# Kernel optimization log

Hardware: AMD Instinct MI355X
Metric: run time of the kernel (lower is better)

The kernel has to match this reference:

```python
import jax, jax.numpy as jnp
import numpy as np

OCC_THRESHOLD = 0.5  # occupancy-bitfield stand-in: cell occupied if grid value > 0.5
T_CLAMP = 1e10


def setup_inputs() -> dict:
    key = jax.random.key(0)
    k1, k2, k3 = jax.random.split(key, 3)
    R = 65536
    # origins inside the scene box [-1,1]^3 (uniform in [-0.5,0.5]^3)
    rays_o = jax.random.uniform(k1, (R, 3), dtype=jnp.float32) - 0.5
    d = jax.random.normal(k2, (R, 3), dtype=jnp.float32)
    rays_d = d / jnp.linalg.norm(d, axis=-1, keepdims=True)
    aabb = jnp.array([[-1.0, -1.0, -1.0], [1.0, 1.0, 1.0]], dtype=jnp.float32)
    density_grid = jax.random.uniform(k3, (1, 128, 128, 128), dtype=jnp.float32)
    return {"rays_o": rays_o, "rays_d": rays_d, "aabb": aabb,
            "density_grid": density_grid, "num_samples": 128}


def reference(rays_o, rays_d, aabb, density_grid, num_samples):
    R = rays_o.shape[0]
    S = int(num_samples)
    aabb_min, aabb_max = aabb[0], aabb[1]

    # ---- ray-AABB intersection (slab test), matching nerfactory_cuda.ray_aabb_intersect ----
    inv_d = 1.0 / rays_d
    t0 = (aabb_min - rays_o) * inv_d  # [R,3]
    t1 = (aabb_max - rays_o) * inv_d
    tn = jnp.max(jnp.minimum(t0, t1), axis=-1)
    tf = jnp.min(jnp.maximum(t0, t1), axis=-1)
    tn = jnp.maximum(tn, 0.0)
    miss = tf <= tn
    t_min = jnp.minimum(jnp.where(miss, T_CLAMP, tn), T_CLAMP)  # [R]
    t_max = jnp.minimum(jnp.where(miss, T_CLAMP, tf), T_CLAMP)  # [R]

    # ---- raymarching: S uniform steps in [t_min, t_max], keep occupied cells ----
    dt = jnp.where(miss, 0.0, (t_max - t_min) / S)  # [R]
    i = jnp.arange(S, dtype=rays_o.dtype)
    starts = t_min[:, None] + i * dt[:, None]        # [R,S]
    ends = starts + dt[:, None]
    t_mid = 0.5 * (starts + ends)
    pos = rays_o[:, None, :] + rays_d[:, None, :] * t_mid[..., None]  # [R,S,3]

    res = density_grid.shape[-1]
    u = (pos - aabb_min) / (aabb_max - aabb_min)  # normalized [0,1]
    cell = jnp.clip(jnp.floor(u * res).astype(jnp.int32), 0, res - 1)
    occ = density_grid[0, cell[..., 0], cell[..., 1], cell[..., 2]] > OCC_THRESHOLD
    valid = occ & (~miss[:, None]) & (dt[:, None] > 0)  # [R,S]

    # ---- stream compaction into packed buffer (fixed capacity R*S) ----
    total = R * S
    flat_valid = valid.reshape(-1)
    excl = jnp.cumsum(flat_valid.astype(jnp.int32)) - flat_valid.astype(jnp.int32)
    scatter_idx = jnp.where(flat_valid, excl, total)  # invalid -> dummy slot

    origins_b = jnp.broadcast_to(rays_o[:, None, :], (R, S, 3))
    dirs_b = jnp.broadcast_to(rays_d[:, None, :], (R, S, 3))
    vals = jnp.concatenate(
        [origins_b, dirs_b, starts[..., None], ends[..., None]], axis=-1
    ).reshape(total, 8)
    packed = jnp.zeros((total + 1, 8), dtype=vals.dtype).at[scatter_idx].set(vals)[:total]

    counts = valid.sum(axis=-1).astype(jnp.int32)        # samples per ray
    ray_start = jnp.cumsum(counts) - counts              # exclusive cumsum
    packed_info = jnp.stack([ray_start, counts], axis=-1)  # [R,2]

    # packed columns: origins(0:3), dirs(3:6), starts(6), ends(7)
    return packed, packed_info, t_min, t_max
```

## Files before the change

### kernel.cpp

```cpp
#include <hip/hip_runtime.h>

#define SAMPLES 128
#define GRID_RES 128

typedef unsigned long long u64;

__device__ __forceinline__ void slab_test(
    float ox, float oy, float oz, float dx, float dy, float dz,
    float a0, float a1, float a2, float b0, float b1, float b2,
    float& tmin, float& tmax, float& dtv, bool& miss)
{
    float ix = __fdiv_rn(1.0f, dx);
    float iy = __fdiv_rn(1.0f, dy);
    float iz = __fdiv_rn(1.0f, dz);
    float t0x = __fmul_rn(__fsub_rn(a0, ox), ix);
    float t1x = __fmul_rn(__fsub_rn(b0, ox), ix);
    float t0y = __fmul_rn(__fsub_rn(a1, oy), iy);
    float t1y = __fmul_rn(__fsub_rn(b1, oy), iy);
    float t0z = __fmul_rn(__fsub_rn(a2, oz), iz);
    float t1z = __fmul_rn(__fsub_rn(b2, oz), iz);
    float tn = fmaxf(fmaxf(fminf(t0x, t1x), fminf(t0y, t1y)), fminf(t0z, t1z));
    float tf = fminf(fminf(fmaxf(t0x, t1x), fmaxf(t0y, t1y)), fmaxf(t0z, t1z));
    tn = fmaxf(tn, 0.0f);
    miss = (tf <= tn);
    tmin = miss ? 1e10f : fminf(tn, 1e10f);
    tmax = miss ? 1e10f : fminf(tf, 1e10f);
    dtv  = miss ? 0.0f : __fmul_rn(__fsub_rn(tmax, tmin), 0.0078125f);
}

__global__ __launch_bounds__(256) void k_prep(
    const float* __restrict__ grid, u64* __restrict__ bits,
    const float* __restrict__ ro, const float* __restrict__ rd,
    const float* __restrict__ aabb,
    float* __restrict__ out_tmin, float* __restrict__ out_tmax,
    float* __restrict__ wtmin, float* __restrict__ wdt,
    unsigned* __restrict__ ctr, int R, int nbb)
{
    int b = blockIdx.x;
    int tid = threadIdx.x;
    if (b < nbb) {
        int m = b * 256 + tid;
        int BZ = m & 31, BY = (m >> 5) & 31, BX = m >> 10;
        u64 word = 0;
        #pragma unroll
        for (int i = 0; i < 4; ++i) {
            #pragma unroll
            for (int j = 0; j < 4; ++j) {
                const float4 v = *(const float4*)(
                    grid + (((size_t)(BX * 4 + i) * GRID_RES + (BY * 4 + j))
                            * GRID_RES + BZ * 4));
                int base = (i << 4) | (j << 2);
                if (v.x > 0.5f) word |= (1ull << (base + 0));
                if (v.y > 0.5f) word |= (1ull << (base + 1));
                if (v.z > 0.5f) word |= (1ull << (base + 2));
                if (v.w > 0.5f) word |= (1ull << (base + 3));
            }
        }
        bits[m] = word;
        return;
    }
    int r = (b - nbb) * 256 + tid;
    if (b == nbb && tid == 0) *ctr = 0u;
    if (r >= R) return;
    float ox = ro[3 * r + 0], oy = ro[3 * r + 1], oz = ro[3 * r + 2];
    float dx = rd[3 * r + 0], dy = rd[3 * r + 1], dz = rd[3 * r + 2];
    float a0 = aabb[0], a1 = aabb[1], a2 = aabb[2];
    float b0 = aabb[3], b1 = aabb[4], b2 = aabb[5];
    float tmin, tmax, dtv; bool miss;
    slab_test(ox, oy, oz, dx, dy, dz, a0, a1, a2, b0, b1, b2,
              tmin, tmax, dtv, miss);
    out_tmin[r] = tmin;
    out_tmax[r] = tmax;
    wtmin[r] = tmin;
    wdt[r]  = dtv;
}

__device__ __forceinline__ float norm_coord(float p, float a, float e)
{
    if (e == 2.0f)
        return __fmul_rn(__fmul_rn(__fsub_rn(p, a), 0.5f), (float)GRID_RES);
    return __fmul_rn(__fdiv_rn(__fsub_rn(p, a), e), (float)GRID_RES);
}

__device__ __forceinline__ bool sample_occ(
    int s, float tmin, float dtv,
    float ox, float oy, float oz, float dx, float dy, float dz,
    float a0, float a1, float a2, float e0, float e1, float e2,
    const u64* __restrict__ bits)
{
    float fs    = (float)s;
    float start = __fadd_rn(tmin, __fmul_rn(fs, dtv));
    float end   = __fadd_rn(start, dtv);
    float tmid  = __fmul_rn(0.5f, __fadd_rn(start, end));
    float px = __fadd_rn(ox, __fmul_rn(dx, tmid));
    float py = __fadd_rn(oy, __fmul_rn(dy, tmid));
    float pz = __fadd_rn(oz, __fmul_rn(dz, tmid));
    float ux = norm_coord(px, a0, e0);
    float uy = norm_coord(py, a1, e1);
    float uz = norm_coord(pz, a2, e2);
    int cx = min(max((int)floorf(ux), 0), GRID_RES - 1);
    int cy = min(max((int)floorf(uy), 0), GRID_RES - 1);
    int cz = min(max((int)floorf(uz), 0), GRID_RES - 1);
    int m  = (((cx >> 2) << 5) | (cy >> 2)) * 32 + (cz >> 2);
    int bb = ((cx & 3) << 4) | ((cy & 3) << 2) | (cz & 3);
    return (bits[m] >> bb) & 1ull;
}

__global__ __launch_bounds__(256) void k_pass1(
    const float* __restrict__ ro, const float* __restrict__ rd,
    const float* __restrict__ aabb, const u64* __restrict__ bits,
    const float* __restrict__ wtmin, const float* __restrict__ wdt,
    u64* __restrict__ wmask, int R)
{
    int tid  = threadIdx.x;
    int lane = tid & 63;
    int ray  = blockIdx.x * 4 + (tid >> 6);
    if (ray >= R) return;
    int rayu = __builtin_amdgcn_readfirstlane(ray);

    float tmin = wtmin[rayu];
    float dtv  = wdt[rayu];

    bool vlo = false, vhi = false;
    if (dtv > 0.0f) {
        float ox = ro[3 * rayu + 0], oy = ro[3 * rayu + 1], oz = ro[3 * rayu + 2];
        float dx = rd[3 * rayu + 0], dy = rd[3 * rayu + 1], dz = rd[3 * rayu + 2];
        float a0 = aabb[0], a1 = aabb[1], a2 = aabb[2];
        float e0 = __fsub_rn(aabb[3], a0);
        float e1 = __fsub_rn(aabb[4], a1);
        float e2 = __fsub_rn(aabb[5], a2);
        vlo = sample_occ(lane,      tmin, dtv, ox, oy, oz, dx, dy, dz,
                         a0, a1, a2, e0, e1, e2, bits);
        vhi = sample_occ(lane + 64, tmin, dtv, ox, oy, oz, dx, dy, dz,
                         a0, a1, a2, e0, e1, e2, bits);
    }

    u64 mlo = __ballot(vlo);
    u64 mhi = __ballot(vhi);
    if (lane == 0) {
        ulonglong2 v; v.x = mlo; v.y = mhi;
        *(ulonglong2*)&wmask[(size_t)ray * 2] = v;
    }
}

__global__ __launch_bounds__(1024) void k_scan(
    const u64* __restrict__ wmask, unsigned* __restrict__ lpre,
    unsigned* __restrict__ bsum, unsigned* __restrict__ boff,
    unsigned* __restrict__ wtotal, unsigned* __restrict__ ctr,
    int R, int nb)
{
    int r    = blockIdx.x * 1024 + threadIdx.x;
    int lane = threadIdx.x & 63;
    int wv   = threadIdx.x >> 6;

    unsigned c = 0;
    if (r < R)
        c = (unsigned)__popcll(wmask[2 * r]) + (unsigned)__popcll(wmask[2 * r + 1]);

    unsigned inc = c;
    for (int o = 1; o < 64; o <<= 1) {
        unsigned v = __shfl_up(inc, o, 64);
        if (lane >= o) inc += v;
    }

    __shared__ unsigned sw[16];
    __shared__ unsigned sdone;
    if (lane == 63) sw[wv] = inc;
    __syncthreads();
    if (wv == 0) {
        unsigned v = (lane < 16) ? sw[lane] : 0u;
        unsigned iv = v;
        for (int o = 1; o < 16; o <<= 1) {
            unsigned t2 = __shfl_up(iv, o, 64);
            if (lane >= o) iv += t2;
        }
        if (lane < 16) sw[lane] = iv - v;
    }
    __syncthreads();

    unsigned excl = sw[wv] + (inc - c);
    if (r < R) lpre[r] = excl;

    if (threadIdx.x == 1023) {
        atomicExch(&bsum[blockIdx.x], excl + c);
        __threadfence();
        sdone = atomicAdd(ctr, 1u);
    }
    __syncthreads();
    if (sdone == (unsigned)(nb - 1)) {
        __threadfence();
        if (threadIdx.x < 64) {
            int t = threadIdx.x;
            unsigned v = (t < nb) ? atomicAdd(&bsum[t], 0u) : 0u;
            unsigned iv = v;
            for (int o = 1; o < 64; o <<= 1) {
                unsigned u = __shfl_up(iv, o, 64);
                if (t >= o) iv += u;
            }
            if (t < nb) boff[t] = iv - v;
            if (t == 63) *wtotal = iv;
        }
    }
}

__global__ __launch_bounds__(256) void k_pack(
    const float* __restrict__ ro, const float* __restrict__ rd,
    const u64* __restrict__ wmask,
    const unsigned* __restrict__ lpre, const unsigned* __restrict__ boff,
    const float* __restrict__ wtmin, const float* __restrict__ wdt,
    const unsigned* __restrict__ wtotal,
    float* __restrict__ packed, float* __restrict__ info, int R)
{
    __shared__ unsigned sbuf[4][64 * 9];

    int tid  = threadIdx.x;
    int wv   = tid >> 6;
    int lane = tid & 63;
    int gid  = blockIdx.x * 256 + tid;
    int ray  = gid >> 7;
    int s    = gid & 127;
    int s0   = s & 64;
    int rayu = __builtin_amdgcn_readfirstlane(ray);

    u64 mlo = wmask[2 * rayu];
    u64 mhi = wmask[2 * rayu + 1];
    u64 mw  = s0 ? mhi : mlo;
    unsigned nv = (unsigned)__popcll(mw);
    unsigned wave_below = (unsigned)__popcll(mw & ((1ull << lane) - 1ull));
    bool valid = (mw >> lane) & 1ull;
    unsigned rank = valid ? wave_below : nv + ((unsigned)lane - wave_below);

    unsigned wstart = boff[rayu >> 10] + lpre[rayu];
    unsigned vbase  = wstart + (s0 ? (unsigned)__popcll(mlo) : 0u);
    unsigned wtot   = *wtotal;
    unsigned gid0   = (unsigned)(gid - lane);
    unsigned tbase  = wtot + gid0 - vbase;

    if (s == 0) {
        unsigned cnt = (unsigned)__popcll(mlo) + (unsigned)__popcll(mhi);
        info[2 * ray]     = (float)wstart;
        info[2 * ray + 1] = (float)cnt;
    }

    unsigned d0 = 0u, d1 = 0u, d2 = 0u, d3 = 0u, d4 = 0u, d5 = 0u, d6 = 0u, d7 = 0u;
    if (valid) {
        float tmin  = wtmin[rayu];
        float dtv   = wdt[rayu];
        float fs    = (float)s;
        float start = __fadd_rn(tmin, __fmul_rn(fs, dtv));
        float end   = __fadd_rn(start, dtv);
        d0 = __float_as_uint(ro[3 * rayu + 0]);
        d1 = __float_as_uint(ro[3 * rayu + 1]);
        d2 = __float_as_uint(ro[3 * rayu + 2]);
        d3 = __float_as_uint(rd[3 * rayu + 0]);
        d4 = __float_as_uint(rd[3 * rayu + 1]);
        d5 = __float_as_uint(rd[3 * rayu + 2]);
        d6 = __float_as_uint(start);
        d7 = __float_as_uint(end);
    }
    unsigned* row = &sbuf[wv][rank * 9];
    row[0] = d0; row[1] = d1; row[2] = d2; row[3] = d3;
    row[4] = d4; row[5] = d5; row[6] = d6; row[7] = d7;

    __syncthreads();

    #pragma unroll
    for (int b = 0; b < 2; ++b) {
        unsigned f = (unsigned)(b * 64 + lane);
        unsigned k = f >> 1;
        unsigned p = f & 1u;
        unsigned dest = (k < nv) ? (vbase + k) : (tbase + (k - nv));
        const unsigned* src = &sbuf[wv][k * 9 + p * 4];
        float4 val = make_float4(__uint_as_float(src[0]), __uint_as_float(src[1]),
                                 __uint_as_float(src[2]), __uint_as_float(src[3]));
        *(float4*)(packed + (size_t)dest * 8 + p * 4) = val;
    }
}

extern "C" void kernel_launch(void* const* d_in, const int* in_sizes, int n_in,
                              void* d_out, int out_size, void* d_ws, size_t ws_size,
                              hipStream_t stream)
{
    const float* ro   = (const float*)d_in[0];
    const float* rd   = (const float*)d_in[1];
    const float* aabb = (const float*)d_in[2];
    const float* grid = (const float*)d_in[3];

    int R = in_sizes[0] / 3;
    size_t total = (size_t)R * SAMPLES;
    int nb = (R + 1023) / 1024;
    int nbricks = 32 * 32 * 32;
    int nbb = nbricks / 256;
    int nrb = (R + 255) / 256;

    float* out    = (float*)d_out;
    float* packed = out;
    float* info   = out + total * 8;
    float* otmin  = info + (size_t)2 * R;
    float* otmax  = otmin + R;

    char* w = (char*)d_ws;
    u64* wmask       = (u64*)w;
    float* wtmin     = (float*)(w + (size_t)R * 16);
    float* wdt       = wtmin + R;
    unsigned* lpre   = (unsigned*)(wdt + R);
    unsigned* bsum   = lpre + R;
    unsigned* boff   = bsum + 64;
    unsigned* wtotal = boff + 64;
    unsigned* ctr    = wtotal + 1;
    u64* bits        = (u64*)(wtotal + 63);

    k_prep<<<nbb + nrb, 256, 0, stream>>>(grid, bits, ro, rd, aabb,
                                          otmin, otmax, wtmin, wdt, ctr, R, nbb);
    int b1 = (R + 3) / 4;
    k_pass1<<<b1, 256, 0, stream>>>(ro, rd, aabb, bits, wtmin, wdt, wmask, R);
    k_scan<<<nb, 1024, 0, stream>>>(wmask, lpre, bsum, boff, wtotal, ctr, R, nb);
    int b3 = (int)(total / 256);
    k_pack<<<b3, 256, 0, stream>>>(ro, rd, wmask, lpre, boff, wtmin, wdt,
                                   wtotal, packed, info, R);
}
```

Measured before the change: 75.82 us.

## Fuse occupancy sampling pass with the per-ray count scan kernel

Merges the ray-sampling kernel and the scan kernel into a single launch. Each 1024-thread block now handles 16 rays, one per wave, and computes the ray counts directly from the ballot masks instead of re-reading them. The block sums then feed a last-block decoupled scan over 4096 block totals, with each thread handling four entries. This removes a kernel launch and the round trip of the masks through global memory. In exchange the final single-block scan is larger and there is more atomic-counter traffic across many blocks.

```diff
diff --git a/kernel.cpp b/kernel.cpp
--- a/kernel.cpp
+++ b/kernel.cpp
@@ -106,66 +106,51 @@
     return (bits[m] >> bb) & 1ull;
 }
 
-__global__ __launch_bounds__(256) void k_pass1(
+__global__ __launch_bounds__(1024) void k_pass1(
     const float* __restrict__ ro, const float* __restrict__ rd,
     const float* __restrict__ aabb, const u64* __restrict__ bits,
     const float* __restrict__ wtmin, const float* __restrict__ wdt,
-    u64* __restrict__ wmask, int R)
-{
-    int tid  = threadIdx.x;
-    int lane = tid & 63;
-    int ray  = blockIdx.x * 4 + (tid >> 6);
-    if (ray >= R) return;
-    int rayu = __builtin_amdgcn_readfirstlane(ray);
-
-    float tmin = wtmin[rayu];
-    float dtv  = wdt[rayu];
-
-    bool vlo = false, vhi = false;
-    if (dtv > 0.0f) {
-        float ox = ro[3 * rayu + 0], oy = ro[3 * rayu + 1], oz = ro[3 * rayu + 2];
-        float dx = rd[3 * rayu + 0], dy = rd[3 * rayu + 1], dz = rd[3 * rayu + 2];
-        float a0 = aabb[0], a1 = aabb[1], a2 = aabb[2];
-        float e0 = __fsub_rn(aabb[3], a0);
-        float e1 = __fsub_rn(aabb[4], a1);
-        float e2 = __fsub_rn(aabb[5], a2);
-        vlo = sample_occ(lane,      tmin, dtv, ox, oy, oz, dx, dy, dz,
-                         a0, a1, a2, e0, e1, e2, bits);
-        vhi = sample_occ(lane + 64, tmin, dtv, ox, oy, oz, dx, dy, dz,
-                         a0, a1, a2, e0, e1, e2, bits);
-    }
-
-    u64 mlo = __ballot(vlo);
-    u64 mhi = __ballot(vhi);
-    if (lane == 0) {
-        ulonglong2 v; v.x = mlo; v.y = mhi;
-        *(ulonglong2*)&wmask[(size_t)ray * 2] = v;
-    }
-}
-
-__global__ __launch_bounds__(1024) void k_scan(
-    const u64* __restrict__ wmask, unsigned* __restrict__ lpre,
+    u64* __restrict__ wmask, unsigned* __restrict__ lpre,
     unsigned* __restrict__ bsum, unsigned* __restrict__ boff,
     unsigned* __restrict__ wtotal, unsigned* __restrict__ ctr,
     int R, int nb)
 {
-    int r    = blockIdx.x * 1024 + threadIdx.x;
-    int lane = threadIdx.x & 63;
-    int wv   = threadIdx.x >> 6;
+    int tid  = threadIdx.x;
+    int lane = tid & 63;
+    int wv   = tid >> 6;
+    int ray  = blockIdx.x * 16 + wv;
+    bool act = (ray < R);
 
     unsigned c = 0;
-    if (r < R)
-        c = (unsigned)__popcll(wmask[2 * r]) + (unsigned)__popcll(wmask[2 * r + 1]);
-
-    unsigned inc = c;
-    for (int o = 1; o < 64; o <<= 1) {
-        unsigned v = __shfl_up(inc, o, 64);
-        if (lane >= o) inc += v;
+    if (act) {
+        int rayu = __builtin_amdgcn_readfirstlane(ray);
+        float tmin = wtmin[rayu];
+        float dtv  = wdt[rayu];
+        bool vlo = false, vhi = false;
+        if (dtv > 0.0f) {
+            float ox = ro[3 * rayu + 0], oy = ro[3 * rayu + 1], oz = ro[3 * rayu + 2];
+            float dx = rd[3 * rayu + 0], dy = rd[3 * rayu + 1], dz = rd[3 * rayu + 2];
+            float a0 = aabb[0], a1 = aabb[1], a2 = aabb[2];
+            float e0 = __fsub_rn(aabb[3], a0);
+            float e1 = __fsub_rn(aabb[4], a1);
+            float e2 = __fsub_rn(aabb[5], a2);
+            vlo = sample_occ(lane,      tmin, dtv, ox, oy, oz, dx, dy, dz,
+                             a0, a1, a2, e0, e1, e2, bits);
+            vhi = sample_occ(lane + 64, tmin, dtv, ox, oy, oz, dx, dy, dz,
+                             a0, a1, a2, e0, e1, e2, bits);
+        }
+        u64 mlo = __ballot(vlo);
+        u64 mhi = __ballot(vhi);
+        c = (unsigned)__popcll(mlo) + (unsigned)__popcll(mhi);
+        if (lane == 0) {
+            ulonglong2 v; v.x = mlo; v.y = mhi;
+            *(ulonglong2*)&wmask[(size_t)ray * 2] = v;
+        }
     }
 
     __shared__ unsigned sw[16];
     __shared__ unsigned sdone;
-    if (lane == 63) sw[wv] = inc;
+    if (lane == 0) sw[wv] = c;
     __syncthreads();
     if (wv == 0) {
         unsigned v = (lane < 16) ? sw[lane] : 0u;
@@ -177,29 +162,49 @@
         if (lane < 16) sw[lane] = iv - v;
     }
     __syncthreads();
-
-    unsigned excl = sw[wv] + (inc - c);
-    if (r < R) lpre[r] = excl;
-
-    if (threadIdx.x == 1023) {
-        atomicExch(&bsum[blockIdx.x], excl + c);
+    if (act && lane == 0) lpre[ray] = sw[wv];
+
+    if (tid == 960) {
+        atomicExch(&bsum[blockIdx.x], sw[15] + c);
         __threadfence();
         sdone = atomicAdd(ctr, 1u);
     }
     __syncthreads();
     if (sdone == (unsigned)(nb - 1)) {
         __threadfence();
-        if (threadIdx.x < 64) {
-            int t = threadIdx.x;
-            unsigned v = (t < nb) ? atomicAdd(&bsum[t], 0u) : 0u;
+        const int per = 4;
+        int base = tid * per;
+        unsigned v0 = 0, v1 = 0, v2 = 0, v3 = 0;
+        if (base + 0 < nb) v0 = atomicAdd(&bsum[base + 0], 0u);
+        if (base + 1 < nb) v1 = atomicAdd(&bsum[base + 1], 0u);
+        if (base + 2 < nb) v2 = atomicAdd(&bsum[base + 2], 0u);
+        if (base + 3 < nb) v3 = atomicAdd(&bsum[base + 3], 0u);
+        unsigned S = v0 + v1 + v2 + v3;
+
+        unsigned inc = S;
+        for (int o = 1; o < 64; o <<= 1) {
+            unsigned t2 = __shfl_up(inc, o, 64);
+            if (lane >= o) inc += t2;
+        }
+        __shared__ unsigned sw2[16];
+        if (lane == 63) sw2[wv] = inc;
+        __syncthreads();
+        if (wv == 0) {
+            unsigned v = (lane < 16) ? sw2[lane] : 0u;
             unsigned iv = v;
-            for (int o = 1; o < 64; o <<= 1) {
-                unsigned u = __shfl_up(iv, o, 64);
-                if (t >= o) iv += u;
+            for (int o = 1; o < 16; o <<= 1) {
+                unsigned t2 = __shfl_up(iv, o, 64);
+                if (lane >= o) iv += t2;
             }
-            if (t < nb) boff[t] = iv - v;
-            if (t == 63) *wtotal = iv;
-        }
+            if (lane < 16) sw2[lane] = iv - v;
+        }
+        __syncthreads();
+        unsigned run = sw2[wv] + (inc - S);
+        if (base + 0 < nb) { boff[base + 0] = run; run += v0; }
+        if (base + 1 < nb) { boff[base + 1] = run; run += v1; }
+        if (base + 2 < nb) { boff[base + 2] = run; run += v2; }
+        if (base + 3 < nb) { boff[base + 3] = run; run += v3; }
+        if (tid == 1023) *wtotal = run;
     }
 }
 
@@ -230,7 +235,7 @@
     bool valid = (mw >> lane) & 1ull;
     unsigned rank = valid ? wave_below : nv + ((unsigned)lane - wave_below);
 
-    unsigned wstart = boff[rayu >> 10] + lpre[rayu];
+    unsigned wstart = boff[rayu >> 4] + lpre[rayu];
     unsigned vbase  = wstart + (s0 ? (unsigned)__popcll(mlo) : 0u);
     unsigned wtot   = *wtotal;
     unsigned gid0   = (unsigned)(gid - lane);
@@ -288,7 +293,7 @@
 
     int R = in_sizes[0] / 3;
     size_t total = (size_t)R * SAMPLES;
-    int nb = (R + 1023) / 1024;
+    int nb1 = (R + 15) / 16;
     int nbricks = 32 * 32 * 32;
     int nbb = nbricks / 256;
     int nrb = (R + 255) / 256;
@@ -305,16 +310,15 @@
     float* wdt       = wtmin + R;
     unsigned* lpre   = (unsigned*)(wdt + R);
     unsigned* bsum   = lpre + R;
-    unsigned* boff   = bsum + 64;
-    unsigned* wtotal = boff + 64;
+    unsigned* boff   = bsum + nb1;
+    unsigned* wtotal = boff + nb1;
     unsigned* ctr    = wtotal + 1;
-    u64* bits        = (u64*)(wtotal + 63);
+    u64* bits        = (u64*)(((uintptr_t)(ctr + 1) + 15) & ~(uintptr_t)15);
 
     k_prep<<<nbb + nrb, 256, 0, stream>>>(grid, bits, ro, rd, aabb,
                                           otmin, otmax, wtmin, wdt, ctr, R, nbb);
-    int b1 = (R + 3) / 4;
-    k_pass1<<<b1, 256, 0, stream>>>(ro, rd, aabb, bits, wtmin, wdt, wmask, R);
-    k_scan<<<nb, 1024, 0, stream>>>(wmask, lpre, bsum, boff, wtotal, ctr, R, nb);
+    k_pass1<<<nb1, 1024, 0, stream>>>(ro, rd, aabb, bits, wtmin, wdt, wmask,
+                                      lpre, bsum, boff, wtotal, ctr, R, nb1);
     int b3 = (int)(total / 256);
     k_pack<<<b3, 256, 0, stream>>>(ro, rd, wmask, lpre, boff, wtmin, wdt,
                                    wtotal, packed, info, R);
```

Result: slower. 170.7 us (+125.2%).
